# Kernel optimization log

Hardware: AMD Instinct MI355X
Metric: run time of the kernel (lower is better)

Reference implementation:

```python
import jax, jax.numpy as jnp
import numpy as np

MIN_SIGMA = 0.1
MAX_SIGMA = 10.0


def _sigma_mlp(e, w1, b1, w2, b2, w3, b3):
    # e: [B, N, E] -> sigma in [min_sigma, max_sigma], shape [B, N, 1]
    h = jax.nn.gelu(e @ w1 + b1, approximate=False)
    h = jax.nn.gelu(h @ w2 + b2, approximate=False)
    s = jax.nn.sigmoid(h @ w3 + b3)
    return MIN_SIGMA + (MAX_SIGMA - MIN_SIGMA) * s


def setup_inputs() -> dict:
    key = jax.random.key(0)
    ks = jax.random.split(key, 9)
    M, P = 2048, 2
    B, N, E = 8, 1024, 256
    H = 32
    z = jax.random.normal(ks[0], (M, P), dtype=jnp.float32)
    mu = jax.random.normal(ks[1], (B, N, P), dtype=jnp.float32)
    embeddings = jax.random.normal(ks[2], (B, N, E), dtype=jnp.float32)
    # sigma-predictor MLP params (torch Linear default-ish init scale)
    w1 = jax.random.normal(ks[3], (E, H), dtype=jnp.float32) / np.sqrt(E)
    b1 = jnp.zeros((H,), dtype=jnp.float32)
    w2 = jax.random.normal(ks[4], (H, H // 2), dtype=jnp.float32) / np.sqrt(H)
    b2 = jnp.zeros((H // 2,), dtype=jnp.float32)
    w3 = jax.random.normal(ks[5], (H // 2, 1), dtype=jnp.float32) / np.sqrt(H // 2)
    b3 = jnp.zeros((1,), dtype=jnp.float32)
    return {"z": z, "mu": mu, "embeddings": embeddings,
            "w1": w1, "b1": b1, "w2": w2, "b2": b2, "w3": w3, "b3": b3}


def reference(z, mu, embeddings, w1, b1, w2, b2, w3, b3):
    # sigma: [B, N, 1]
    sigma = _sigma_mlp(embeddings, w1, b1, w2, b2, w3, b3)
    # squared distances: [B, N, M] = sum_P (z[m,p] - mu[b,n,p])^2
    # z: [M, P], mu: [B, N, P]
    d2 = jnp.sum((z[None, None, :, :] - mu[:, :, None, :]) ** 2, axis=-1)
    # kernel values: [B, N, M]
    return jnp.exp(-d2 / (2.0 * sigma ** 2))
```

## Files before the change

kernel.cpp:

```cpp
#include <hip/hip_runtime.h>
#include <math.h>

#define ROWS 8192
#define M_TOTAL 2048
#define E_DIM 256
#define H1 32
#define H2 16
#define R_PER_BLK 32

__device__ __forceinline__ float gelu_exact(float x) {
    return 0.5f * x * (1.0f + erff(x * 0.70710678118654752f));
}

__global__ __launch_bounds__(256) void sigma_mlp_v2(
    const float* __restrict__ emb,
    const float* __restrict__ w1, const float* __restrict__ b1,
    const float* __restrict__ w2, const float* __restrict__ b2,
    const float* __restrict__ w3, const float* __restrict__ b3,
    float* __restrict__ c_out)
{
    __shared__ float se[R_PER_BLK * E_DIM];
    __shared__ float sw1[E_DIM * H1];
    __shared__ float sh1[R_PER_BLK][H1 + 1];
    __shared__ float sh2[R_PER_BLK][H2 + 1];

    const int t = threadIdx.x;
    const int row0 = blockIdx.x * R_PER_BLK;

    {
        const float4* src_e = (const float4*)(emb + (size_t)row0 * E_DIM);
        float4* dst_e = (float4*)se;
        const float4* src_w = (const float4*)w1;
        float4* dst_w = (float4*)sw1;
        #pragma unroll
        for (int i = 0; i < 8; ++i) {
            dst_e[t + 256 * i] = src_e[t + 256 * i];
            dst_w[t + 256 * i] = src_w[t + 256 * i];
        }
    }
    __syncthreads();

    {
        const int o = t & 31;
        const int g = t >> 5;
        float acc0 = 0.f, acc1 = 0.f, acc2 = 0.f, acc3 = 0.f;
        const float4* se4 = (const float4*)se;
        const int rb = g * 4;
        for (int k4 = 0; k4 < E_DIM / 4; ++k4) {
            float4 e0 = se4[(rb + 0) * (E_DIM / 4) + k4];
            float4 e1 = se4[(rb + 1) * (E_DIM / 4) + k4];
            float4 e2 = se4[(rb + 2) * (E_DIM / 4) + k4];
            float4 e3 = se4[(rb + 3) * (E_DIM / 4) + k4];
            const int k = k4 * 4;
            float wa = sw1[(k + 0) * H1 + o];
            float wb = sw1[(k + 1) * H1 + o];
            float wc = sw1[(k + 2) * H1 + o];
            float wd = sw1[(k + 3) * H1 + o];
            acc0 = fmaf(e0.x, wa, acc0); acc0 = fmaf(e0.y, wb, acc0);
            acc0 = fmaf(e0.z, wc, acc0); acc0 = fmaf(e0.w, wd, acc0);
            acc1 = fmaf(e1.x, wa, acc1); acc1 = fmaf(e1.y, wb, acc1);
            acc1 = fmaf(e1.z, wc, acc1); acc1 = fmaf(e1.w, wd, acc1);
            acc2 = fmaf(e2.x, wa, acc2); acc2 = fmaf(e2.y, wb, acc2);
            acc2 = fmaf(e2.z, wc, acc2); acc2 = fmaf(e2.w, wd, acc2);
            acc3 = fmaf(e3.x, wa, acc3); acc3 = fmaf(e3.y, wb, acc3);
            acc3 = fmaf(e3.z, wc, acc3); acc3 = fmaf(e3.w, wd, acc3);
        }
        const float bo = b1[o];
        sh1[rb + 0][o] = gelu_exact(acc0 + bo);
        sh1[rb + 1][o] = gelu_exact(acc1 + bo);
        sh1[rb + 2][o] = gelu_exact(acc2 + bo);
        sh1[rb + 3][o] = gelu_exact(acc3 + bo);
    }
    __syncthreads();

    {
        const int o2 = t & 15;
        const int rr = t >> 4;
        const float bo = b2[o2];
        #pragma unroll
        for (int h = 0; h < 2; ++h) {
            const int r = rr + 16 * h;
            float a = 0.f;
            #pragma unroll
            for (int k = 0; k < H1; ++k) a = fmaf(sh1[r][k], w2[k * H2 + o2], a);
            sh2[r][o2] = gelu_exact(a + bo);
        }
    }
    __syncthreads();

    if (t < R_PER_BLK) {
        float s = 0.f;
        #pragma unroll
        for (int k = 0; k < H2; ++k) s = fmaf(sh2[t][k], w3[k], s);
        const float x = s + b3[0];
        const float sig = 1.0f / (1.0f + __expf(-x));
        const float sigma = 0.1f + 9.9f * sig;
        c_out[row0 + t] = -0.5f / (sigma * sigma);
    }
}

__global__ __launch_bounds__(256) void rbf_kernel(
    const float* __restrict__ z, const float* __restrict__ mu,
    const float* __restrict__ c_in, float* __restrict__ out)
{
    const int row = blockIdx.x;
    const int t = threadIdx.x;
    const float c = c_in[row];
    const float mu0 = mu[row * 2 + 0];
    const float mu1 = mu[row * 2 + 1];
    const float4* zf4 = (const float4*)z;
    float4* out4 = (float4*)out + (size_t)row * (M_TOTAL / 4);

    #pragma unroll
    for (int i = 0; i < 2; ++i) {
        const int idx = i * 256 + t;
        const float4 za = zf4[idx * 2 + 0];
        const float4 zb = zf4[idx * 2 + 1];
        float4 r;
        float d0, d1;
        d0 = za.x - mu0; d1 = za.y - mu1;
        r.x = __expf(fmaf(d1, d1, d0 * d0) * c);
        d0 = za.z - mu0; d1 = za.w - mu1;
        r.y = __expf(fmaf(d1, d1, d0 * d0) * c);
        d0 = zb.x - mu0; d1 = zb.y - mu1;
        r.z = __expf(fmaf(d1, d1, d0 * d0) * c);
        d0 = zb.z - mu0; d1 = zb.w - mu1;
        r.w = __expf(fmaf(d1, d1, d0 * d0) * c);
        out4[idx] = r;
    }
}

extern "C" void kernel_launch(void* const* d_in, const int* in_sizes, int n_in,
                              void* d_out, int out_size, void* d_ws, size_t ws_size,
                              hipStream_t stream) {
    const float* z   = (const float*)d_in[0];
    const float* mu  = (const float*)d_in[1];
    const float* emb = (const float*)d_in[2];
    const float* w1  = (const float*)d_in[3];
    const float* b1  = (const float*)d_in[4];
    const float* w2  = (const float*)d_in[5];
    const float* b2  = (const float*)d_in[6];
    const float* w3  = (const float*)d_in[7];
    const float* b3  = (const float*)d_in[8];
    float* out = (float*)d_out;
    float* c_ws = (float*)d_ws;

    sigma_mlp_v2<<<ROWS / R_PER_BLK, 256, 0, stream>>>(emb, w1, b1, w2, b2, w3, b3, c_ws);
    rbf_kernel<<<ROWS, 256, 0, stream>>>(z, mu, c_ws, out);
}
```

Baseline: 106.6 us.

## Fuse sigma MLP into RBF kernel with one row per block

Merges the two kernels into one. Each block computes its row's sigma MLP: the first layer is split across all 256 threads as partial float4 dot products, then reduced in shared memory. The squared distances are computed before the MLP so the z loads overlap with it. This removes the second launch, the workspace round trip and the under-occupied MLP kernel, which ran only 256 blocks. In exchange, every block re-reads the full 32KB w1 matrix from cache, and the layer-2 and layer-3 steps rely on wave-level ordering rather than barriers.

```diff
diff --git a/kernel.cpp b/kernel.cpp
--- a/kernel.cpp
+++ b/kernel.cpp
@@ -6,126 +6,97 @@
 #define E_DIM 256
 #define H1 32
 #define H2 16
-#define R_PER_BLK 32
 
 __device__ __forceinline__ float gelu_exact(float x) {
     return 0.5f * x * (1.0f + erff(x * 0.70710678118654752f));
 }
 
-__global__ __launch_bounds__(256) void sigma_mlp_v2(
+__global__ __launch_bounds__(256) void fused_rbf(
+    const float* __restrict__ z, const float* __restrict__ mu,
     const float* __restrict__ emb,
     const float* __restrict__ w1, const float* __restrict__ b1,
     const float* __restrict__ w2, const float* __restrict__ b2,
     const float* __restrict__ w3, const float* __restrict__ b3,
-    float* __restrict__ c_out)
+    float* __restrict__ out)
 {
-    __shared__ float se[R_PER_BLK * E_DIM];
-    __shared__ float sw1[E_DIM * H1];
-    __shared__ float sh1[R_PER_BLK][H1 + 1];
-    __shared__ float sh2[R_PER_BLK][H2 + 1];
+    __shared__ __align__(16) float sh1p[32 * 32];
+    __shared__ float sh1[H1];
+    __shared__ float sh2[H2];
+    __shared__ float sc;
 
     const int t = threadIdx.x;
-    const int row0 = blockIdx.x * R_PER_BLK;
+    const int row = blockIdx.x;
 
-    {
-        const float4* src_e = (const float4*)(emb + (size_t)row0 * E_DIM);
-        float4* dst_e = (float4*)se;
-        const float4* src_w = (const float4*)w1;
-        float4* dst_w = (float4*)sw1;
-        #pragma unroll
-        for (int i = 0; i < 8; ++i) {
-            dst_e[t + 256 * i] = src_e[t + 256 * i];
-            dst_w[t + 256 * i] = src_w[t + 256 * i];
-        }
-    }
-    __syncthreads();
-
-    {
-        const int o = t & 31;
-        const int g = t >> 5;
-        float acc0 = 0.f, acc1 = 0.f, acc2 = 0.f, acc3 = 0.f;
-        const float4* se4 = (const float4*)se;
-        const int rb = g * 4;
-        for (int k4 = 0; k4 < E_DIM / 4; ++k4) {
-            float4 e0 = se4[(rb + 0) * (E_DIM / 4) + k4];
-            float4 e1 = se4[(rb + 1) * (E_DIM / 4) + k4];
-            float4 e2 = se4[(rb + 2) * (E_DIM / 4) + k4];
-            float4 e3 = se4[(rb + 3) * (E_DIM / 4) + k4];
-            const int k = k4 * 4;
-            float wa = sw1[(k + 0) * H1 + o];
-            float wb = sw1[(k + 1) * H1 + o];
-            float wc = sw1[(k + 2) * H1 + o];
-            float wd = sw1[(k + 3) * H1 + o];
-            acc0 = fmaf(e0.x, wa, acc0); acc0 = fmaf(e0.y, wb, acc0);
-            acc0 = fmaf(e0.z, wc, acc0); acc0 = fmaf(e0.w, wd, acc0);
-            acc1 = fmaf(e1.x, wa, acc1); acc1 = fmaf(e1.y, wb, acc1);
-            acc1 = fmaf(e1.z, wc, acc1); acc1 = fmaf(e1.w, wd, acc1);
-            acc2 = fmaf(e2.x, wa, acc2); acc2 = fmaf(e2.y, wb, acc2);
-            acc2 = fmaf(e2.z, wc, acc2); acc2 = fmaf(e2.w, wd, acc2);
-            acc3 = fmaf(e3.x, wa, acc3); acc3 = fmaf(e3.y, wb, acc3);
-            acc3 = fmaf(e3.z, wc, acc3); acc3 = fmaf(e3.w, wd, acc3);
-        }
-        const float bo = b1[o];
-        sh1[rb + 0][o] = gelu_exact(acc0 + bo);
-        sh1[rb + 1][o] = gelu_exact(acc1 + bo);
-        sh1[rb + 2][o] = gelu_exact(acc2 + bo);
-        sh1[rb + 3][o] = gelu_exact(acc3 + bo);
-    }
-    __syncthreads();
-
-    {
-        const int o2 = t & 15;
-        const int rr = t >> 4;
-        const float bo = b2[o2];
-        #pragma unroll
-        for (int h = 0; h < 2; ++h) {
-            const int r = rr + 16 * h;
-            float a = 0.f;
-            #pragma unroll
-            for (int k = 0; k < H1; ++k) a = fmaf(sh1[r][k], w2[k * H2 + o2], a);
-            sh2[r][o2] = gelu_exact(a + bo);
-        }
-    }
-    __syncthreads();
-
-    if (t < R_PER_BLK) {
-        float s = 0.f;
-        #pragma unroll
-        for (int k = 0; k < H2; ++k) s = fmaf(sh2[t][k], w3[k], s);
-        const float x = s + b3[0];
-        const float sig = 1.0f / (1.0f + __expf(-x));
-        const float sigma = 0.1f + 9.9f * sig;
-        c_out[row0 + t] = -0.5f / (sigma * sigma);
-    }
-}
-
-__global__ __launch_bounds__(256) void rbf_kernel(
-    const float* __restrict__ z, const float* __restrict__ mu,
-    const float* __restrict__ c_in, float* __restrict__ out)
-{
-    const int row = blockIdx.x;
-    const int t = threadIdx.x;
-    const float c = c_in[row];
     const float mu0 = mu[row * 2 + 0];
     const float mu1 = mu[row * 2 + 1];
     const float4* zf4 = (const float4*)z;
-    float4* out4 = (float4*)out + (size_t)row * (M_TOTAL / 4);
-
+    float d2[8];
     #pragma unroll
     for (int i = 0; i < 2; ++i) {
         const int idx = i * 256 + t;
         const float4 za = zf4[idx * 2 + 0];
         const float4 zb = zf4[idx * 2 + 1];
+        float a, b;
+        a = za.x - mu0; b = za.y - mu1; d2[i * 4 + 0] = fmaf(b, b, a * a);
+        a = za.z - mu0; b = za.w - mu1; d2[i * 4 + 1] = fmaf(b, b, a * a);
+        a = zb.x - mu0; b = zb.y - mu1; d2[i * 4 + 2] = fmaf(b, b, a * a);
+        a = zb.z - mu0; b = zb.w - mu1; d2[i * 4 + 3] = fmaf(b, b, a * a);
+    }
+
+    {
+        const int og = t & 7;
+        const int kg = t >> 3;
+        const float4* e4 = (const float4*)(emb + (size_t)row * E_DIM);
+        const float4 e0 = e4[kg * 2 + 0];
+        const float4 e1 = e4[kg * 2 + 1];
+        const float ev[8] = {e0.x, e0.y, e0.z, e0.w, e1.x, e1.y, e1.z, e1.w};
+        const float4* w14 = (const float4*)w1;
+        float4 p = make_float4(0.f, 0.f, 0.f, 0.f);
+        #pragma unroll
+        for (int kk = 0; kk < 8; ++kk) {
+            const float4 w = w14[(kg * 8 + kk) * 8 + og];
+            p.x = fmaf(ev[kk], w.x, p.x);
+            p.y = fmaf(ev[kk], w.y, p.y);
+            p.z = fmaf(ev[kk], w.z, p.z);
+            p.w = fmaf(ev[kk], w.w, p.w);
+        }
+        ((float4*)sh1p)[t] = p;
+    }
+    __syncthreads();
+
+    if (t < H1) {
+        float a = 0.f;
+        #pragma unroll
+        for (int kg = 0; kg < 32; ++kg) a += sh1p[kg * 32 + t];
+        sh1[t] = gelu_exact(a + b1[t]);
+    }
+    if (t < H2) {
+        float a = 0.f;
+        #pragma unroll
+        for (int k = 0; k < H1; ++k) a = fmaf(sh1[k], w2[k * H2 + t], a);
+        sh2[t] = gelu_exact(a + b2[t]);
+    }
+    if (t == 0) {
+        float s = 0.f;
+        #pragma unroll
+        for (int k = 0; k < H2; ++k) s = fmaf(sh2[k], w3[k], s);
+        const float x = s + b3[0];
+        const float sig = 1.0f / (1.0f + __expf(-x));
+        const float sigma = 0.1f + 9.9f * sig;
+        sc = -0.5f / (sigma * sigma);
+    }
+    __syncthreads();
+
+    const float c = sc;
+    float4* out4 = (float4*)out + (size_t)row * (M_TOTAL / 4);
+    #pragma unroll
+    for (int i = 0; i < 2; ++i) {
+        const int idx = i * 256 + t;
         float4 r;
-        float d0, d1;
-        d0 = za.x - mu0; d1 = za.y - mu1;
-        r.x = __expf(fmaf(d1, d1, d0 * d0) * c);
-        d0 = za.z - mu0; d1 = za.w - mu1;
-        r.y = __expf(fmaf(d1, d1, d0 * d0) * c);
-        d0 = zb.x - mu0; d1 = zb.y - mu1;
-        r.z = __expf(fmaf(d1, d1, d0 * d0) * c);
-        d0 = zb.z - mu0; d1 = zb.w - mu1;
-        r.w = __expf(fmaf(d1, d1, d0 * d0) * c);
+        r.x = __expf(d2[i * 4 + 0] * c);
+        r.y = __expf(d2[i * 4 + 1] * c);
+        r.z = __expf(d2[i * 4 + 2] * c);
+        r.w = __expf(d2[i * 4 + 3] * c);
         out4[idx] = r;
     }
 }
@@ -143,8 +114,6 @@
     const float* w3  = (const float*)d_in[7];
     const float* b3  = (const float*)d_in[8];
     float* out = (float*)d_out;
-    float* c_ws = (float*)d_ws;
 
-    sigma_mlp_v2<<<ROWS / R_PER_BLK, 256, 0, stream>>>(emb, w1, b1, w2, b2, w3, b3, c_ws);
-    rbf_kernel<<<ROWS, 256, 0, stream>>>(z, mu, c_ws, out);
+    fused_rbf<<<ROWS, 256, 0, stream>>>(z, mu, emb, w1, b1, w2, b2, w3, b3, out);
 }
```

After: 108.7 us. Within noise of the previous version (+2.0%).
